# Kernel tuning notes

Measured on AMD Instinct MI355X. Metric: run time of the kernel, lower is better.

## Reference

```python
import jax, jax.numpy as jnp
import numpy as np

# angular momenta of the full basis (2s,3s,2p,3p,3d) -> block sizes 1,1,3,3,5; norb=13
L_LIST = [0, 0, 1, 1, 2]


def factor_matrix():
    """Replicates the orbital-pair loop: factor 0.5 on diagonal orbital blocks,
    1.0 for i<j blocks, 0.0 below the block diagonal (only i<=j filled)."""
    sizes = [2 * l + 1 for l in L_LIST]
    norb = sum(sizes)
    F = np.zeros((norb, norb), np.float32)
    ist = 0
    for i, si in enumerate(sizes):
        jst = 0
        for j, sj in enumerate(sizes):
            if i < j:
                F[ist:ist + si, jst:jst + sj] = 1.0
            elif i == j:
                F[ist:ist + si, jst:jst + sj] = 0.5
            jst += sj
        ist += si
    return jnp.asarray(F)


def setup_inputs() -> dict:
    key = jax.random.key(0)
    k1, k2, k3, k4, k5 = jax.random.split(key, 5)
    N, E, K = 128, 2048, 16
    norb = sum(2 * l + 1 for l in L_LIST)  # 13
    return {
        "hopping": jax.random.normal(k1, (E, norb * norb), jnp.float32),
        "onsite": jax.random.normal(k2, (N, norb * norb), jnp.float32),
        "kpoints": jax.random.uniform(k3, (K, 3), jnp.float32),
        "cell_shift": jax.random.normal(k4, (E, 3), jnp.float32),
        "edge_index": jax.random.randint(k5, (2, E), 0, N, jnp.int64),
    }


def reference(hopping, onsite, kpoints, cell_shift, edge_index):
    F = factor_matrix()
    norb = F.shape[0]
    N = onsite.shape[0]
    K = kpoints.shape[0]
    ctype = jnp.complex64

    # per-edge / per-atom orbital blocks with upper-triangular factor (i<=j loop)
    hop = (hopping.reshape(-1, norb, norb) * F).astype(ctype)   # [E,norb,norb]
    ons = (onsite.reshape(-1, norb, norb) * F).astype(ctype)    # [N,norb,norb]

    # Bloch phase exp(-i 2*pi k.R) per (k, edge)
    phase = jnp.exp(-1j * 2.0 * jnp.pi * (kpoints @ cell_shift.T).astype(ctype))  # [K,E]

    # assemble block Hamiltonian [K, N, N, norb, norb]
    H = jnp.zeros((K, N, N, norb, norb), ctype)
    ar = jnp.arange(N)
    H = H.at[:, ar, ar].add(ons[None])  # onsite diagonal blocks (no phase)
    ie, je = edge_index[0], edge_index[1]
    H = H.at[:, ie, je].add(phase[:, :, None, None] * hop[None])  # scatter-add edges

    # hermitize: block + block^H (swap atom blocks and orbital indices)
    H = H + jnp.conj(jnp.swapaxes(jnp.swapaxes(H, 1, 2), 3, 4))
    # [K, N, norb, N, norb] -> [K, all_norb, all_norb]
    Hk = H.transpose(0, 1, 3, 2, 4).reshape(K, N * norb, N * norb)
    return Hk
```

## Files before the change

### kernel.cpp

```cpp
#include <hip/hip_runtime.h>
#include <math.h>

#define NORB 13
#define NORB2 (NORB * NORB)
#define NTHR 256
#define MAXE 256
#define NBIN 128

typedef float fx2 __attribute__((ext_vector_type(2)));
typedef float fx4 __attribute__((ext_vector_type(4)));

__device__ __forceinline__ int blk_of(int p) {
    return p < 1 ? 0 : (p < 2 ? 1 : (p < 5 ? 2 : (p < 8 ? 3 : 4)));
}
__device__ __forceinline__ float bfac(int bp, int bq) {
    return bp < bq ? 1.0f : (bp == bq ? 0.5f : 0.0f);
}

__global__ void __launch_bounds__(NTHR)
k_fused(const float* __restrict__ hopping,
        const float* __restrict__ onsite,
        const float* __restrict__ kpoints,
        const float* __restrict__ cell_shift,
        const int* __restrict__ edge_index,
        float* __restrict__ out,
        int N, int E, int K, int ld, int es) {
    int a = blockIdx.x % N;
    int k = blockIdx.x / N;
    int tid = threadIdx.x;

    __shared__ int   boff[NBIN + 1];
    __shared__ int   cur[NBIN];
    __shared__ int   elist[MAXE];
    __shared__ float phc[MAXE];
    __shared__ float phs[MAXE];

    if (tid < NBIN) boff[tid] = 0;
    __syncthreads();

    for (int e = tid; e < E; e += NTHR) {
        int ie = edge_index[e], je = edge_index[E + e];
        if (ie == a) atomicAdd(&boff[je], 1);
        if (je == a) atomicAdd(&boff[ie], 1);
    }
    __syncthreads();

    if (tid < 64) {
        int v0 = boff[2 * tid], v1 = boff[2 * tid + 1];
        int s = v0 + v1, sc = s;
        #pragma unroll
        for (int d = 1; d < 64; d <<= 1) {
            int t = __shfl_up(sc, d);
            if (tid >= d) sc += t;
        }
        int excl = sc - s;
        boff[2 * tid] = excl;       cur[2 * tid] = excl;
        boff[2 * tid + 1] = excl + v0; cur[2 * tid + 1] = excl + v0;
        if (tid == 63) boff[NBIN] = sc;
    }
    __syncthreads();

    for (int e = tid; e < E; e += NTHR) {
        int ie = edge_index[e], je = edge_index[E + e];
        if (ie == a) {
            int pos = atomicAdd(&cur[je], 1);
            if (pos < MAXE) elist[pos] = (e << 8) | (je << 1);
        }
        if (je == a) {
            int pos = atomicAdd(&cur[ie], 1);
            if (pos < MAXE) elist[pos] = (e << 8) | (ie << 1) | 1;
        }
    }
    __syncthreads();
    int nent = min(boff[NBIN], MAXE);

    float kx = kpoints[3 * k], ky = kpoints[3 * k + 1], kz = kpoints[3 * k + 2];
    for (int t = tid; t < nent; t += NTHR) {
        int ent = elist[t];
        int e = ent >> 8;
        float d = kx * cell_shift[3 * e] + ky * cell_shift[3 * e + 1]
                + kz * cell_shift[3 * e + 2];
        float s, c;
        __sincosf(-6.2831853071795864f * d, &s, &c);
        phc[t] = c;
        phs[t] = (ent & 1) ? -s : s;
    }
    __syncthreads();

    const float* on = onsite + (size_t)a * NORB2;
    size_t rb = (size_t)(k * ld + a * NORB) * ld;
    int nch = (ld + 511) >> 9;

    #pragma unroll 1
    for (int p = 0; p < NORB; ++p) {
        int bp = blk_of(p);
        #pragma unroll 1
        for (int ch = 0; ch < nch; ++ch) {
            int c0 = (ch << 9) + 2 * tid;
            if (c0 >= ld) continue;
            float vx[2], vy[2];
            #pragma unroll
            for (int u = 0; u < 2; ++u) {
                int c = c0 + u;
                int b = c / NORB, q = c - NORB * b;
                int bq = blk_of(q);
                float fpq = bfac(bp, bq), fqp = bfac(bq, bp);
                float ax = 0.f, ay = 0.f;
                if (b == a)
                    ax = on[p * NORB + q] * fpq + on[q * NORB + p] * fqp;
                int i0 = boff[b], i1 = boff[b + 1];
                if (i1 > MAXE) i1 = MAXE;
                for (int it = i0; it < i1; ++it) {
                    int ent = elist[it];
                    const float* h = hopping + (size_t)(ent >> 8) * NORB2;
                    float hv = (ent & 1) ? h[q * NORB + p] * fqp
                                         : h[p * NORB + q] * fpq;
                    ax += phc[it] * hv;
                    ay += phs[it] * hv;
                }
                vx[u] = ax; vy[u] = ay;
            }
            size_t ci = rb + (size_t)p * ld + c0;
            if (es == 2) {
                ((fx4*)out)[ci >> 1] = (fx4){vx[0], vy[0], vx[1], vy[1]};
            } else {
                ((fx2*)out)[ci >> 1] = (fx2){vx[0], vx[1]};
            }
        }
    }
}

extern "C" void kernel_launch(void* const* d_in, const int* in_sizes, int n_in,
                              void* d_out, int out_size, void* d_ws, size_t ws_size,
                              hipStream_t stream) {
    const float* hopping    = (const float*)d_in[0];
    const float* onsite     = (const float*)d_in[1];
    const float* kpoints    = (const float*)d_in[2];
    const float* cell_shift = (const float*)d_in[3];
    const int*   edge_index = (const int*)d_in[4];
    float* out = (float*)d_out;

    int E = in_sizes[0] / NORB2;
    int N = in_sizes[1] / NORB2;
    int K = in_sizes[2] / 3;
    int ld = N * NORB;

    size_t full = (size_t)K * ld * ld * 2;
    int es = ((size_t)out_size >= full) ? 2 : 1;

    int nwg = N * K;
    k_fused<<<nwg, NTHR, 0, stream>>>(hopping, onsite, kpoints, cell_shift,
                                      edge_index, out, N, E, K, ld, es);
}
```

Before: 239.6 us.

## Split dense zero-fill from sparse nonzero-block computation

Adds a separate vectorised zero-fill kernel for the whole output. The Hamiltonian kernel then computes only the orbital blocks of atoms that share edges with the row atom (plus the onsite block), using a compacted list of nonzero neighbour blocks. This is meant to remove the per-column index arithmetic and neighbour-range checks spent on the many all-zero entries. It costs an extra kernel launch and scattered small stores for the nonzero entries.

```diff
diff --git a/kernel.cpp b/kernel.cpp
--- a/kernel.cpp
+++ b/kernel.cpp
@@ -6,6 +6,7 @@
 #define NTHR 256
 #define MAXE 256
 #define NBIN 128
+#define MAXB 129
 
 typedef float fx2 __attribute__((ext_vector_type(2)));
 typedef float fx4 __attribute__((ext_vector_type(4)));
@@ -18,13 +19,22 @@
 }
 
 __global__ void __launch_bounds__(NTHR)
-k_fused(const float* __restrict__ hopping,
-        const float* __restrict__ onsite,
-        const float* __restrict__ kpoints,
-        const float* __restrict__ cell_shift,
-        const int* __restrict__ edge_index,
-        float* __restrict__ out,
-        int N, int E, int K, int ld, int es) {
+k_zero(float* __restrict__ out, size_t nfx4) {
+    size_t i = (size_t)blockIdx.x * NTHR + threadIdx.x;
+    size_t stride = (size_t)gridDim.x * NTHR;
+    fx4* o = (fx4*)out;
+    fx4 z = (fx4){0.f, 0.f, 0.f, 0.f};
+    for (; i < nfx4; i += stride) o[i] = z;
+}
+
+__global__ void __launch_bounds__(NTHR)
+k_sparse(const float* __restrict__ hopping,
+         const float* __restrict__ onsite,
+         const float* __restrict__ kpoints,
+         const float* __restrict__ cell_shift,
+         const int* __restrict__ edge_index,
+         float* __restrict__ out,
+         int N, int E, int K, int ld, int es) {
     int a = blockIdx.x % N;
     int k = blockIdx.x / N;
     int tid = threadIdx.x;
@@ -34,8 +44,11 @@
     __shared__ int   elist[MAXE];
     __shared__ float phc[MAXE];
     __shared__ float phs[MAXE];
+    __shared__ int   nzb[MAXB];
+    __shared__ int   nnz;
 
     if (tid < NBIN) boff[tid] = 0;
+    if (tid == 0) nnz = 0;
     __syncthreads();
 
     for (int e = tid; e < E; e += NTHR) {
@@ -54,7 +67,7 @@
             if (tid >= d) sc += t;
         }
         int excl = sc - s;
-        boff[2 * tid] = excl;       cur[2 * tid] = excl;
+        boff[2 * tid] = excl;          cur[2 * tid] = excl;
         boff[2 * tid + 1] = excl + v0; cur[2 * tid + 1] = excl + v0;
         if (tid == 63) boff[NBIN] = sc;
     }
@@ -85,48 +98,45 @@
         phc[t] = c;
         phs[t] = (ent & 1) ? -s : s;
     }
+
+    if (tid < NBIN) {
+        int i0 = boff[tid];
+        int i1 = boff[tid + 1]; if (i1 > MAXE) i1 = MAXE;
+        if (i1 > i0 || tid == a) {
+            int s = atomicAdd(&nnz, 1);
+            nzb[s] = tid | (i0 << 7) | (i1 << 16);
+        }
+    }
     __syncthreads();
+    int nb = nnz;
 
     const float* on = onsite + (size_t)a * NORB2;
     size_t rb = (size_t)(k * ld + a * NORB) * ld;
-    int nch = (ld + 511) >> 9;
 
-    #pragma unroll 1
-    for (int p = 0; p < NORB; ++p) {
-        int bp = blk_of(p);
-        #pragma unroll 1
-        for (int ch = 0; ch < nch; ++ch) {
-            int c0 = (ch << 9) + 2 * tid;
-            if (c0 >= ld) continue;
-            float vx[2], vy[2];
-            #pragma unroll
-            for (int u = 0; u < 2; ++u) {
-                int c = c0 + u;
-                int b = c / NORB, q = c - NORB * b;
-                int bq = blk_of(q);
-                float fpq = bfac(bp, bq), fqp = bfac(bq, bp);
-                float ax = 0.f, ay = 0.f;
-                if (b == a)
-                    ax = on[p * NORB + q] * fpq + on[q * NORB + p] * fqp;
-                int i0 = boff[b], i1 = boff[b + 1];
-                if (i1 > MAXE) i1 = MAXE;
-                for (int it = i0; it < i1; ++it) {
-                    int ent = elist[it];
-                    const float* h = hopping + (size_t)(ent >> 8) * NORB2;
-                    float hv = (ent & 1) ? h[q * NORB + p] * fqp
-                                         : h[p * NORB + q] * fpq;
-                    ax += phc[it] * hv;
-                    ay += phs[it] * hv;
-                }
-                vx[u] = ax; vy[u] = ay;
-            }
-            size_t ci = rb + (size_t)p * ld + c0;
-            if (es == 2) {
-                ((fx4*)out)[ci >> 1] = (fx4){vx[0], vy[0], vx[1], vy[1]};
-            } else {
-                ((fx2*)out)[ci >> 1] = (fx2){vx[0], vx[1]};
-            }
+    int tot = nb * NORB2;
+    for (int idx = tid; idx < tot; idx += NTHR) {
+        int blk = idx / NORB2;
+        int r   = idx - blk * NORB2;
+        int p = r / NORB, q = r - p * NORB;
+        int info = nzb[blk];
+        int b  = info & 127;
+        int i0 = (info >> 7) & 511, i1 = (info >> 16) & 511;
+        int bp = blk_of(p), bq = blk_of(q);
+        float fpq = bfac(bp, bq), fqp = bfac(bq, bp);
+        float ax = 0.f, ay = 0.f;
+        if (b == a)
+            ax = on[p * NORB + q] * fpq + on[q * NORB + p] * fqp;
+        for (int it = i0; it < i1; ++it) {
+            int ent = elist[it];
+            const float* h = hopping + (size_t)(ent >> 8) * NORB2;
+            float hv = (ent & 1) ? h[q * NORB + p] * fqp
+                                 : h[p * NORB + q] * fpq;
+            ax += phc[it] * hv;
+            ay += phs[it] * hv;
         }
+        size_t ci = rb + (size_t)p * ld + (size_t)b * NORB + q;
+        if (es == 2) ((fx2*)out)[ci] = (fx2){ax, ay};
+        else         out[ci] = ax;
     }
 }
 
@@ -147,8 +157,11 @@
 
     size_t full = (size_t)K * ld * ld * 2;
     int es = ((size_t)out_size >= full) ? 2 : 1;
+    size_t nfloats = (size_t)K * ld * ld * (es == 2 ? 2 : 1);
+
+    k_zero<<<8192, NTHR, 0, stream>>>(out, nfloats / 4);
 
     int nwg = N * K;
-    k_fused<<<nwg, NTHR, 0, stream>>>(hopping, onsite, kpoints, cell_shift,
-                                      edge_index, out, N, E, K, ld, es);
+    k_sparse<<<nwg, NTHR, 0, stream>>>(hopping, onsite, kpoints, cell_shift,
+                                       edge_index, out, N, E, K, ld, es);
 }
```

Result: faster. 230.9 us (-3.7%).
